# Kernel optimization log

Hardware: AMD Instinct MI355X
Metric: run time of the kernel (lower is better)

## Reference

```python
import jax, jax.numpy as jnp
import numpy as np

B, T, D, H, L, F = 128, 512, 32, 128, 3, 4


def setup_inputs() -> dict:
    key = jax.random.key(0)
    ks = jax.random.split(key, 13)
    s = 0.05
    inp = {
        "x": jax.random.normal(ks[0], (B, T, D), dtype=jnp.float32),
        # layer 0 input weights [4H, D]; layers 1..L-1 input weights [L-1, 4H, H]
        "w_ih0": jax.random.normal(ks[1], (4 * H, D), dtype=jnp.float32) * s,
        "w_ih_rest": jax.random.normal(ks[2], (L - 1, 4 * H, H), dtype=jnp.float32) * s,
        "w_hh": jax.random.normal(ks[3], (L, 4 * H, H), dtype=jnp.float32) * s,
        "b_ih": jax.random.normal(ks[4], (L, 4 * H), dtype=jnp.float32) * s,
        "b_hh": jax.random.normal(ks[5], (L, 4 * H), dtype=jnp.float32) * s,
        "w_attn": jax.random.normal(ks[6], (1, H), dtype=jnp.float32) * s,
        "b_attn": jax.random.normal(ks[7], (1,), dtype=jnp.float32) * s,
        "w1": jax.random.normal(ks[8], (64, H), dtype=jnp.float32) * s,
        "b1": jax.random.normal(ks[9], (64,), dtype=jnp.float32) * s,
        "w2": jax.random.normal(ks[10], (F, 64), dtype=jnp.float32) * s,
        "b2": jax.random.normal(ks[11], (F,), dtype=jnp.float32) * s,
    }
    return inp


def _lstm_layer(xs, w_ih, w_hh, bi, bh):
    # xs: [B, T, Din] -> hs: [B, T, H]; PyTorch gate order i, f, g, o
    b, t = xs.shape[0], xs.shape[1]
    h_dim = w_hh.shape[1]
    pre = jnp.einsum('bti,gi->btg', xs, w_ih) + bi + bh  # [B, T, 4H]

    def step(carry, p_t):
        h, c = carry
        g = p_t + h @ w_hh.T
        i, f, gg, o = jnp.split(g, 4, axis=-1)
        i = jax.nn.sigmoid(i)
        f = jax.nn.sigmoid(f)
        gg = jnp.tanh(gg)
        o = jax.nn.sigmoid(o)
        c = f * c + i * gg
        h = o * jnp.tanh(c)
        return (h, c), h

    h0 = jnp.zeros((b, h_dim), xs.dtype)
    _, hs = jax.lax.scan(step, (h0, h0), jnp.swapaxes(pre, 0, 1))
    return jnp.swapaxes(hs, 0, 1)


def reference(x, w_ih0, w_ih_rest, w_hh, b_ih, b_hh, w_attn, b_attn, w1, b1, w2, b2):
    out = _lstm_layer(x, w_ih0, w_hh[0], b_ih[0], b_hh[0])
    for l in range(1, L):
        out = _lstm_layer(out, w_ih_rest[l - 1], w_hh[l], b_ih[l], b_hh[l])
    # additive attention pooling over time
    attn_w = jax.nn.softmax(jnp.einsum('bth,oh->bto', out, w_attn) + b_attn, axis=1)  # [B,T,1]
    ctx = jnp.sum(attn_w * out, axis=1)  # [B, H]
    # MLP head (dropout is identity at inference)
    h1 = jax.nn.relu(ctx @ w1.T + b1)
    return h1 @ w2.T + b2
```

## Files before the change

kernel.cpp:

```cpp
#include <hip/hip_runtime.h>
#include <math.h>

#define Bn 128
#define Tn 512
#define Dn 32
#define Hn 128
#define Gn 512
#define Ln 3

#define BAR_LDS() asm volatile("s_waitcnt lgkmcnt(0)\n\ts_barrier" ::: "memory")

typedef _Float16 h2 __attribute__((ext_vector_type(2)));
typedef _Float16 half8 __attribute__((ext_vector_type(8)));
typedef float f32x4 __attribute__((ext_vector_type(4)));

__device__ __forceinline__ float dot2(h2 a, h2 b, float c) {
    return __builtin_amdgcn_fdot2(a, b, c, false);
}
__device__ __forceinline__ h2 pkh(float a, float b) {
    h2 r; r.x = (_Float16)a; r.y = (_Float16)b; return r;
}
__device__ __forceinline__ float sigm(float x) {
    return __builtin_amdgcn_rcpf(1.f + __expf(-x));
}
__device__ __forceinline__ float tanh_fast(float x) {
    return 1.f - 2.f * __builtin_amdgcn_rcpf(1.f + __expf(2.f * x));
}

#define DPPADD(a, CTRL) { \
    int _t = __builtin_amdgcn_update_dpp(0, __builtin_bit_cast(int, a), \
                                         CTRL, 0xF, 0xF, true); \
    a += __builtin_bit_cast(float, _t); }

#define KEEPH(x) asm volatile("" : "+v"(x))
#define LD8H(p) (*(const half8*)(p))
#define H2OF(V, i) (((const h2*)&(V))[i])

#define DECL16(P, R) \
  h2 P##0=pkh((R)[0],(R)[1]),   P##1=pkh((R)[2],(R)[3]),   P##2=pkh((R)[4],(R)[5]),   P##3=pkh((R)[6],(R)[7]),   \
     P##4=pkh((R)[8],(R)[9]),   P##5=pkh((R)[10],(R)[11]), P##6=pkh((R)[12],(R)[13]), P##7=pkh((R)[14],(R)[15]), \
     P##8=pkh((R)[16],(R)[17]), P##9=pkh((R)[18],(R)[19]), P##10=pkh((R)[20],(R)[21]),P##11=pkh((R)[22],(R)[23]),\
     P##12=pkh((R)[24],(R)[25]),P##13=pkh((R)[26],(R)[27]),P##14=pkh((R)[28],(R)[29]),P##15=pkh((R)[30],(R)[31]);
#define KEEP16(P) \
  KEEPH(P##0); KEEPH(P##1); KEEPH(P##2); KEEPH(P##3); KEEPH(P##4); KEEPH(P##5); \
  KEEPH(P##6); KEEPH(P##7); KEEPH(P##8); KEEPH(P##9); KEEPH(P##10); KEEPH(P##11); \
  KEEPH(P##12); KEEPH(P##13); KEEPH(P##14); KEEPH(P##15);

#define EXTRACT16(P, A, B, C, D) \
  h2 P##0 = H2OF(A,0), P##1 = H2OF(A,1), P##2  = H2OF(A,2), P##3  = H2OF(A,3), \
     P##4 = H2OF(B,0), P##5 = H2OF(B,1), P##6  = H2OF(B,2), P##7  = H2OF(B,3), \
     P##8 = H2OF(C,0), P##9 = H2OF(C,1), P##10 = H2OF(C,2), P##11 = H2OF(C,3), \
     P##12= H2OF(D,0), P##13= H2OF(D,1), P##14 = H2OF(D,2), P##15 = H2OF(D,3);

#define DOTA(j) { \
    aI = dot2(hvA##j, wiA##j, aI);  aF = dot2(hvA##j, wfA##j, aF); \
    aG = dot2(hvA##j, wgA##j, aG);  aO = dot2(hvA##j, woA##j, aO); }
#define DOTB(j) { \
    aI = dot2(hvB##j, wiB##j, aI);  aF = dot2(hvB##j, wfB##j, aF); \
    aG = dot2(hvB##j, wgB##j, aG);  aO = dot2(hvB##j, woB##j, aO); }

template<typename TA>
__global__ __launch_bounds__(256) void gemm_pre(
    const TA* __restrict__ A, int K, int rowStrideB, int t0, int tlog,
    const float* __restrict__ W,
    const float* __restrict__ bi, const float* __restrict__ bh,
    _Float16* __restrict__ C)
{
    __shared__ h2 As2[64][20];
    __shared__ h2 Bs2[64][20];
    const int tid  = threadIdx.x;
    const int row0 = blockIdx.x * 64;
    const int col0 = blockIdx.y * 64;
    const int w    = tid >> 6;
    const int lane = tid & 63;
    const int qm   = (w >> 1) * 32;
    const int qn   = (w & 1) * 32;
    const int fm   = lane & 15;
    const int fq   = lane >> 4;
    const int tmask = (1 << tlog) - 1;
    const int lrow = tid >> 2;
    const int lk   = (tid & 3) * 8;

    f32x4 acc00 = {0,0,0,0}, acc01 = {0,0,0,0};
    f32x4 acc10 = {0,0,0,0}, acc11 = {0,0,0,0};

    for (int k0 = 0; k0 < K; k0 += 32) {
        {
            int rg = row0 + lrow;
            int b_idx = rg >> tlog, tt = rg & tmask;
            const TA* ap = A + (size_t)b_idx * rowStrideB +
                           (size_t)(t0 + tt) * K + (k0 + lk);
            if constexpr (sizeof(TA) == 2) {
                *(float4*)&As2[lrow][(tid & 3) * 4] = *(const float4*)ap;
            } else {
                float4 va = *(const float4*)ap;
                float4 vb = *(const float4*)(ap + 4);
                float4 o;
                ((h2*)&o)[0] = pkh(va.x, va.y);
                ((h2*)&o)[1] = pkh(va.z, va.w);
                ((h2*)&o)[2] = pkh(vb.x, vb.y);
                ((h2*)&o)[3] = pkh(vb.z, vb.w);
                *(float4*)&As2[lrow][(tid & 3) * 4] = o;
            }
            const float* wp = W + (size_t)(col0 + lrow) * K + (k0 + lk);
            float4 wa = *(const float4*)wp;
            float4 wb = *(const float4*)(wp + 4);
            float4 ow;
            ((h2*)&ow)[0] = pkh(wa.x, wa.y);
            ((h2*)&ow)[1] = pkh(wa.z, wa.w);
            ((h2*)&ow)[2] = pkh(wb.x, wb.y);
            ((h2*)&ow)[3] = pkh(wb.z, wb.w);
            *(float4*)&Bs2[lrow][(tid & 3) * 4] = ow;
        }
        __syncthreads();
        half8 a0 = *(const half8*)&As2[qm + fm][fq * 4];
        half8 a1 = *(const half8*)&As2[qm + 16 + fm][fq * 4];
        half8 b0 = *(const half8*)&Bs2[qn + fm][fq * 4];
        half8 b1 = *(const half8*)&Bs2[qn + 16 + fm][fq * 4];
        acc00 = __builtin_amdgcn_mfma_f32_16x16x32_f16(a0, b0, acc00, 0, 0, 0);
        acc01 = __builtin_amdgcn_mfma_f32_16x16x32_f16(a0, b1, acc01, 0, 0, 0);
        acc10 = __builtin_amdgcn_mfma_f32_16x16x32_f16(a1, b0, acc10, 0, 0, 0);
        acc11 = __builtin_amdgcn_mfma_f32_16x16x32_f16(a1, b1, acc11, 0, 0, 0);
        __syncthreads();
    }

    const int g0 = col0 + qn + fm;
    const int g1 = g0 + 16;
    const float bb0 = bi[g0] + bh[g0];
    const float bb1 = bi[g1] + bh[g1];
    const int m0 = row0 + qm + fq * 4;
    #pragma unroll
    for (int r = 0; r < 4; r++) {
        int ma = m0 + r, mb = m0 + 16 + r;
        C[((size_t)(ma >> 1) * Gn + g0) * 2 + (ma & 1)] = (_Float16)(acc00[r] + bb0);
        C[((size_t)(ma >> 1) * Gn + g1) * 2 + (ma & 1)] = (_Float16)(acc01[r] + bb1);
        C[((size_t)(mb >> 1) * Gn + g0) * 2 + (mb & 1)] = (_Float16)(acc10[r] + bb0);
        C[((size_t)(mb >> 1) * Gn + g1) * 2 + (mb & 1)] = (_Float16)(acc11[r] + bb1);
    }
}

__global__ __launch_bounds__(256)
__attribute__((amdgpu_waves_per_eu(1, 2)))
void scan256(
    const _Float16* __restrict__ pre,
    const float* __restrict__ w_hh,
    _Float16* __restrict__ hs16)
{
    const int b    = blockIdx.x;
    const int tid  = threadIdx.x;
    const int lane = tid & 63;
    const int wv   = tid >> 6;
    const int kq   = lane & 1;
    const int u    = wv * 32 + (lane >> 1);

    __shared__ h2 hbuf[2][Hn / 2];
    __shared__ float lds_pad[20480];

    if (pre == nullptr) {
        lds_pad[tid] = (float)tid;
        __syncthreads();
        ((float*)hs16)[tid] = lds_pad[(tid * 7) & 20479];
    }

    const float* rI = w_hh + (size_t)(0 * Hn + u) * Hn + kq * 64;
    const float* rF = w_hh + (size_t)(1 * Hn + u) * Hn + kq * 64;
    const float* rG = w_hh + (size_t)(2 * Hn + u) * Hn + kq * 64;
    const float* rO = w_hh + (size_t)(3 * Hn + u) * Hn + kq * 64;
    DECL16(wiA, rI) DECL16(wiB, (rI + 32))
    DECL16(wfA, rF) DECL16(wfB, (rF + 32))
    DECL16(wgA, rG) DECL16(wgB, (rG + 32))
    DECL16(woA, rO) DECL16(woB, (rO + 32))
    KEEP16(wiA) KEEP16(wiB) KEEP16(wfA) KEEP16(wfB)
    KEEP16(wgA) KEEP16(wgB) KEEP16(woA) KEEP16(woB)

    if (tid < Hn / 2) hbuf[0][tid] = pkh(0.f, 0.f);
    __syncthreads();

    const h2* qq = (const h2*)pre + (size_t)(b * 256) * Gn + u;
    _Float16* hswr = hs16 + (size_t)b * Tn * Hn + u;

    const float ms = (kq == 0) ? 1.f : 0.f;

    h2 qI0 = qq[0],        qF0 = qq[128],      qG0 = qq[256],      qO0 = qq[384];
    h2 qI1 = qq[Gn],       qF1 = qq[Gn + 128], qG1 = qq[Gn + 256], qO1 = qq[Gn + 384];
    const h2* pld = qq + 2 * (size_t)Gn;

    float cr = 0.f;

    auto body = [&](int t, float vI, float vF, float vG, float vO) {
        const h2* hrow = &hbuf[t & 1][kq * 32];
        half8 hA = LD8H(hrow);      half8 hB = LD8H(hrow + 4);
        half8 hC = LD8H(hrow + 8);  half8 hD = LD8H(hrow + 12);
        half8 hE = LD8H(hrow + 16); half8 hF_ = LD8H(hrow + 20);
        half8 hG_ = LD8H(hrow + 24); half8 hH_ = LD8H(hrow + 28);
        EXTRACT16(hvA, hA, hB, hC, hD)
        EXTRACT16(hvB, hE, hF_, hG_, hH_)

        float aI = vI, aF = vF, aG = vG, aO = vO;
        DOTA(0)  DOTA(1)  DOTA(2)  DOTA(3)
        DOTA(4)  DOTA(5)  DOTA(6)  DOTA(7)
        DOTA(8)  DOTA(9)  DOTA(10) DOTA(11)
        DOTA(12) DOTA(13) DOTA(14) DOTA(15)
        DOTB(0)  DOTB(1)  DOTB(2)  DOTB(3)
        DOTB(4)  DOTB(5)  DOTB(6)  DOTB(7)
        DOTB(8)  DOTB(9)  DOTB(10) DOTB(11)
        DOTB(12) DOTB(13) DOTB(14) DOTB(15)

        DPPADD(aI, 0xB1) DPPADD(aF, 0xB1) DPPADD(aG, 0xB1) DPPADD(aO, 0xB1)

        float iv = sigm(aI);
        float fv = sigm(aF);
        float gv = tanh_fast(aG);
        float ov = sigm(aO);
        cr = fv * cr + iv * gv;
        float hnew = ov * tanh_fast(cr);
        _Float16 hh = (_Float16)hnew;
        if (kq == 0) {
            ((_Float16*)hbuf[(t + 1) & 1])[u] = hh;
            *hswr = hh;
        }
        hswr += Hn;
        BAR_LDS();
    };

    for (int pr = 0; pr < 254; pr++) {
        body(2 * pr,     ms * (float)qI0.x, ms * (float)qF0.x,
                         ms * (float)qG0.x, ms * (float)qO0.x);
        body(2 * pr + 1, ms * (float)qI0.y, ms * (float)qF0.y,
                         ms * (float)qG0.y, ms * (float)qO0.y);
        qI0 = qI1; qF0 = qF1; qG0 = qG1; qO0 = qO1;
        qI1 = pld[0]; qF1 = pld[128]; qG1 = pld[256]; qO1 = pld[384];
        pld += Gn;
    }
    body(508, ms * (float)qI0.x, ms * (float)qF0.x,
              ms * (float)qG0.x, ms * (float)qO0.x);
    body(509, ms * (float)qI0.y, ms * (float)qF0.y,
              ms * (float)qG0.y, ms * (float)qO0.y);
    qI0 = qI1; qF0 = qF1; qG0 = qG1; qO0 = qO1;
    body(510, ms * (float)qI0.x, ms * (float)qF0.x,
              ms * (float)qG0.x, ms * (float)qO0.x);
    body(511, ms * (float)qI0.y, ms * (float)qF0.y,
              ms * (float)qG0.y, ms * (float)qO0.y);
}

__global__ __launch_bounds__(256) void head_kernel(
    const _Float16* __restrict__ hs16,
    const float* __restrict__ w_attn, const float* __restrict__ b_attn,
    const float* __restrict__ w1, const float* __restrict__ b1,
    const float* __restrict__ w2, const float* __restrict__ b2,
    float* __restrict__ out)
{
    const int b = blockIdx.x;
    const int tid = threadIdx.x;
    __shared__ h2 wa2[Hn / 2];
    __shared__ __align__(16) float sc[Tn];
    __shared__ __align__(16) float red[256];
    __shared__ __align__(16) float ctx_sh[Hn];
    __shared__ __align__(16) float h1_sh[64];

    if (tid < Hn / 2) wa2[tid] = pkh(w_attn[2 * tid], w_attn[2 * tid + 1]);
    __syncthreads();

    const _Float16* hb = hs16 + (size_t)b * Tn * Hn;

    for (int t = tid; t < Tn; t += 256) {
        const h2* hp = (const h2*)(hb + (size_t)t * Hn);
        float s = 0.f;
        #pragma unroll
        for (int k = 0; k < 64; k++) s = dot2(hp[k], wa2[k], s);
        sc[t] = s + b_attn[0];
    }
    __syncthreads();

    float m = fmaxf(sc[tid], sc[tid + 256]);
    red[tid] = m; __syncthreads();
    for (int s_ = 128; s_ > 0; s_ >>= 1) {
        if (tid < s_) red[tid] = fmaxf(red[tid], red[tid + s_]);
        __syncthreads();
    }
    float mx = red[0];
    __syncthreads();
    float e0 = __expf(sc[tid] - mx), e1 = __expf(sc[tid + 256] - mx);
    sc[tid] = e0; sc[tid + 256] = e1;
    red[tid] = e0 + e1; __syncthreads();
    for (int s_ = 128; s_ > 0; s_ >>= 1) {
        if (tid < s_) red[tid] += red[tid + s_];
        __syncthreads();
    }
    float inv = 1.f / red[0];
    __syncthreads();

    {
        int jj = tid & 127, half = tid >> 7;
        float a = 0.f;
        for (int t = half * 256; t < half * 256 + 256; t++)
            a += sc[t] * (float)hb[(size_t)t * Hn + jj];
        red[tid] = a;
        __syncthreads();
        if (tid < Hn) ctx_sh[tid] = (red[tid] + red[tid + Hn]) * inv;
        __syncthreads();
    }

    if (tid < 64) {
        const float4* wvv = (const float4*)(w1 + (size_t)tid * Hn);
        const float4* cv = (const float4*)ctx_sh;
        float s = 0.f;
        #pragma unroll
        for (int k = 0; k < 32; k++) {
            float4 a = wvv[k], c = cv[k];
            s += a.x * c.x + a.y * c.y + a.z * c.z + a.w * c.w;
        }
        h1_sh[tid] = fmaxf(s + b1[tid], 0.f);
    }
    __syncthreads();

    if (tid < 4) {
        float s = 0.f;
        const float* wvv = w2 + tid * 64;
        #pragma unroll
        for (int k = 0; k < 64; k++) s += wvv[k] * h1_sh[k];
        out[b * 4 + tid] = s + b2[tid];
    }
}

extern "C" void kernel_launch(void* const* d_in, const int* in_sizes, int n_in,
                              void* d_out, int out_size, void* d_ws, size_t ws_size,
                              hipStream_t stream)
{
    const float* x        = (const float*)d_in[0];
    const float* w_ih0    = (const float*)d_in[1];
    const float* w_ih_rest= (const float*)d_in[2];
    const float* w_hh     = (const float*)d_in[3];
    const float* b_ih     = (const float*)d_in[4];
    const float* b_hh     = (const float*)d_in[5];
    const float* w_attn   = (const float*)d_in[6];
    const float* b_attn   = (const float*)d_in[7];
    const float* w1       = (const float*)d_in[8];
    const float* b1       = (const float*)d_in[9];
    const float* w2       = (const float*)d_in[10];
    const float* b2       = (const float*)d_in[11];
    float* out = (float*)d_out;

    const size_t nHS  = (size_t)Bn * Tn * Hn;
    const size_t nPRE = (size_t)Bn * Tn * Gn;

    _Float16* preh = (_Float16*)d_ws;
    _Float16* hs0  = preh + nPRE;
    _Float16* hs1  = hs0 + nHS;
    _Float16* hs2  = hs1 + nHS;

    gemm_pre<float><<<dim3(Bn * Tn / 64, 8), 256, 0, stream>>>(
        x, Dn, Tn * Dn, 0, 9, w_ih0, b_ih, b_hh, preh);
    scan256<<<Bn, 256, 0, stream>>>(preh, w_hh, hs0);

    gemm_pre<_Float16><<<dim3(Bn * Tn / 64, 8), 256, 0, stream>>>(
        hs0, Hn, Tn * Hn, 0, 9, w_ih_rest,
        b_ih + Gn, b_hh + Gn, preh);
    scan256<<<Bn, 256, 0, stream>>>(preh, w_hh + (size_t)Gn * Hn, hs1);

    gemm_pre<_Float16><<<dim3(Bn * Tn / 64, 8), 256, 0, stream>>>(
        hs1, Hn, Tn * Hn, 0, 9, w_ih_rest + (size_t)Gn * Hn,
        b_ih + 2 * Gn, b_hh + 2 * Gn, preh);
    scan256<<<Bn, 256, 0, stream>>>(preh, w_hh + 2 * (size_t)Gn * Hn, hs2);

    head_kernel<<<Bn, 256, 0, stream>>>(hs2, w_attn, b_attn, w1, b1, w2, b2, out);
}
```

Baseline: 1.011 ms.

## Interleave pre-activations by four timesteps and stage hidden outputs in LDS

```diff
diff --git a/kernel.cpp b/kernel.cpp
--- a/kernel.cpp
+++ b/kernel.cpp
@@ -11,6 +11,7 @@
 #define BAR_LDS() asm volatile("s_waitcnt lgkmcnt(0)\n\ts_barrier" ::: "memory")
 
 typedef _Float16 h2 __attribute__((ext_vector_type(2)));
+typedef _Float16 h4 __attribute__((ext_vector_type(4)));
 typedef _Float16 half8 __attribute__((ext_vector_type(8)));
 typedef float f32x4 __attribute__((ext_vector_type(4)));
 
@@ -132,10 +133,10 @@
     #pragma unroll
     for (int r = 0; r < 4; r++) {
         int ma = m0 + r, mb = m0 + 16 + r;
-        C[((size_t)(ma >> 1) * Gn + g0) * 2 + (ma & 1)] = (_Float16)(acc00[r] + bb0);
-        C[((size_t)(ma >> 1) * Gn + g1) * 2 + (ma & 1)] = (_Float16)(acc01[r] + bb1);
-        C[((size_t)(mb >> 1) * Gn + g0) * 2 + (mb & 1)] = (_Float16)(acc10[r] + bb0);
-        C[((size_t)(mb >> 1) * Gn + g1) * 2 + (mb & 1)] = (_Float16)(acc11[r] + bb1);
+        C[((size_t)(ma >> 2) * Gn + g0) * 4 + (ma & 3)] = (_Float16)(acc00[r] + bb0);
+        C[((size_t)(ma >> 2) * Gn + g1) * 4 + (ma & 3)] = (_Float16)(acc01[r] + bb1);
+        C[((size_t)(mb >> 2) * Gn + g0) * 4 + (mb & 3)] = (_Float16)(acc10[r] + bb0);
+        C[((size_t)(mb >> 2) * Gn + g1) * 4 + (mb & 3)] = (_Float16)(acc11[r] + bb1);
     }
 }
 
@@ -154,12 +155,13 @@
     const int u    = wv * 32 + (lane >> 1);
 
     __shared__ h2 hbuf[2][Hn / 2];
-    __shared__ float lds_pad[20480];
+    __shared__ _Float16 hstage[2][16][Hn];
+    __shared__ float lds_pad[19456];
 
     if (pre == nullptr) {
         lds_pad[tid] = (float)tid;
         __syncthreads();
-        ((float*)hs16)[tid] = lds_pad[(tid * 7) & 20479];
+        ((float*)hs16)[tid] = lds_pad[(tid * 7) & 19455];
     }
 
     const float* rI = w_hh + (size_t)(0 * Hn + u) * Hn + kq * 64;
@@ -176,14 +178,14 @@
     if (tid < Hn / 2) hbuf[0][tid] = pkh(0.f, 0.f);
     __syncthreads();
 
-    const h2* qq = (const h2*)pre + (size_t)(b * 256) * Gn + u;
-    _Float16* hswr = hs16 + (size_t)b * Tn * Hn + u;
+    const h4* qq = (const h4*)pre + (size_t)(b * 128) * Gn + u;
+    _Float16* hsb = hs16 + (size_t)b * Tn * Hn;
 
     const float ms = (kq == 0) ? 1.f : 0.f;
 
-    h2 qI0 = qq[0],        qF0 = qq[128],      qG0 = qq[256],      qO0 = qq[384];
-    h2 qI1 = qq[Gn],       qF1 = qq[Gn + 128], qG1 = qq[Gn + 256], qO1 = qq[Gn + 384];
-    const h2* pld = qq + 2 * (size_t)Gn;
+    h4 qI0 = qq[0],   qF0 = qq[128],      qG0 = qq[256],      qO0 = qq[384];
+    h4 qI1 = qq[Gn],  qF1 = qq[Gn + 128], qG1 = qq[Gn + 256], qO1 = qq[Gn + 384];
+    const h4* pld = qq + 2 * (size_t)Gn;
 
     float cr = 0.f;
 
@@ -217,30 +219,49 @@
         _Float16 hh = (_Float16)hnew;
         if (kq == 0) {
             ((_Float16*)hbuf[(t + 1) & 1])[u] = hh;
-            *hswr = hh;
+            hstage[(t >> 4) & 1][t & 15][u] = hh;
         }
-        hswr += Hn;
         BAR_LDS();
     };
 
-    for (int pr = 0; pr < 254; pr++) {
-        body(2 * pr,     ms * (float)qI0.x, ms * (float)qF0.x,
+    auto flush = [&](int ch) {
+        const float4* src = (const float4*)&hstage[ch & 1][0][0];
+        float4 v = src[tid];
+        *(float4*)(hsb + (size_t)ch * 16 * Hn + tid * 8) = v;
+    };
+
+    for (int qr = 0; qr < 126; qr++) {
+        body(4 * qr,     ms * (float)qI0.x, ms * (float)qF0.x,
                          ms * (float)qG0.x, ms * (float)qO0.x);
-        body(2 * pr + 1, ms * (float)qI0.y, ms * (float)qF0.y,
+        body(4 * qr + 1, ms * (float)qI0.y, ms * (float)qF0.y,
                          ms * (float)qG0.y, ms * (float)qO0.y);
+        body(4 * qr + 2, ms * (float)qI0.z, ms * (float)qF0.z,
+                         ms * (float)qG0.z, ms * (float)qO0.z);
+        body(4 * qr + 3, ms * (float)qI0.w, ms * (float)qF0.w,
+                         ms * (float)qG0.w, ms * (float)qO0.w);
+        if ((qr & 3) == 3) flush(qr >> 2);
         qI0 = qI1; qF0 = qF1; qG0 = qG1; qO0 = qO1;
         qI1 = pld[0]; qF1 = pld[128]; qG1 = pld[256]; qO1 = pld[384];
         pld += Gn;
     }
+    body(504, ms * (float)qI0.x, ms * (float)qF0.x,
+              ms * (float)qG0.x, ms * (float)qO0.x);
+    body(505, ms * (float)qI0.y, ms * (float)qF0.y,
+              ms * (float)qG0.y, ms * (float)qO0.y);
+    body(506, ms * (float)qI0.z, ms * (float)qF0.z,
+              ms * (float)qG0.z, ms * (float)qO0.z);
+    body(507, ms * (float)qI0.w, ms * (float)qF0.w,
+              ms * (float)qG0.w, ms * (float)qO0.w);
+    qI0 = qI1; qF0 = qF1; qG0 = qG1; qO0 = qO1;
     body(508, ms * (float)qI0.x, ms * (float)qF0.x,
               ms * (float)qG0.x, ms * (float)qO0.x);
     body(509, ms * (float)qI0.y, ms * (float)qF0.y,
               ms * (float)qG0.y, ms * (float)qO0.y);
-    qI0 = qI1; qF0 = qF1; qG0 = qG1; qO0 = qO1;
-    body(510, ms * (float)qI0.x, ms * (float)qF0.x,
-              ms * (float)qG0.x, ms * (float)qO0.x);
-    body(511, ms * (float)qI0.y, ms * (float)qF0.y,
-              ms * (float)qG0.y, ms * (float)qO0.y);
+    body(510, ms * (float)qI0.z, ms * (float)qF0.z,
+              ms * (float)qG0.z, ms * (float)qO0.z);
+    body(511, ms * (float)qI0.w, ms * (float)qF0.w,
+              ms * (float)qG0.w, ms * (float)qO0.w);
+    flush(31);
 }
 
 __global__ __launch_bounds__(256) void head_kernel(
```

After: 991.3 us. -2.0%, faster.
